# Performance work log

Hardware: AMD Instinct MI355X
Metric: run time of the kernel (lower is better)

Reference implementation:

```python
import jax, jax.numpy as jnp
import numpy as np

N, E, HID, HEADS, KHOPS = 10000, 160000, 64, 8, 3
D = HID // HEADS  # head_dim = 8


def setup_inputs() -> dict:
    key = jax.random.key(0)
    ks = jax.random.split(key, 8)
    s = 1.0 / np.sqrt(HID)
    return {
        "x": jax.random.normal(ks[0], (N, HID), jnp.float32),
        "edge_index": jax.random.randint(ks[1], (2, E), 0, N),
        "edge_feature": jax.random.normal(ks[2], (E, HID), jnp.float32),
        "edge_weight": jax.random.uniform(ks[3], (E,), jnp.float32),
        "Wq": jax.random.normal(ks[4], (HID, HID), jnp.float32) * s,
        "bq": jnp.zeros((HID,), jnp.float32),
        "Wk": jax.random.normal(ks[5], (HID, HID), jnp.float32) * s,
        "bk": jnp.zeros((HID,), jnp.float32),
        "Wv": jax.random.normal(ks[6], (HID, HID), jnp.float32) * s,
        "bv": jnp.zeros((HID,), jnp.float32),
        "hopwise": jnp.ones((KHOPS + 1,), jnp.float32),
    }


def reference(x, edge_index, edge_feature, edge_weight, Wq, bq, Wk, bk, Wv, bv, hopwise):
    n = x.shape[0]
    row, col = edge_index[0], edge_index[1]

    # symmetric degree normalization, scaled by edge_weight
    deg = jax.ops.segment_sum(jnp.ones_like(edge_weight), col, num_segments=n)
    deg_inv = jnp.where(deg > 0, deg ** -0.5, 0.0)
    norm = deg_inv[row] * deg_inv[col] * edge_weight  # [E]

    Q = jax.nn.relu(x @ Wq + bq).reshape(n, HEADS, D)
    K = (x @ Wk + bk).reshape(n, HEADS, D)
    V = (x @ Wv + bv).reshape(n, HEADS, D)
    ef = edge_feature.reshape(-1, HEADS, D)  # [E,h,d]

    hidden = V * hopwise[0]
    sqrt_d = jnp.sqrt(jnp.asarray(D, x.dtype))

    for hop in range(KHOPS):
        if hop == 0:
            Kj = jax.nn.relu(K[row] + ef)                 # [E,h,d]
            # per-edge K (x) V outer product message, scatter-summed at col
            msg = norm[:, None, None, None] * jnp.einsum('ehi,ehj->ehij', Kj, V[row])
            M = jax.ops.segment_sum(msg, col, num_segments=n)   # [N,h,d,d]
            K = jax.ops.segment_sum(norm[:, None, None] * Kj, col, num_segments=n)
        else:
            M = jax.ops.segment_sum(norm[:, None, None, None] * M[row], col, num_segments=n)
            K = jax.ops.segment_sum(norm[:, None, None] * K[row], col, num_segments=n)

        H = jnp.einsum('nhi,nhij->nhj', Q, M)             # [N,h,d]
        nrm = jnp.sqrt(jnp.sum((H / sqrt_d) ** 2, axis=-1))  # [N,h]
        H = H / jnp.maximum(jnp.ones_like(nrm), nrm)[..., None]
        hidden = hidden + hopwise[hop + 1] * H

    return hidden.reshape(n, HEADS * D)
```

## Files before the change

### kernel.cpp

```cpp
#include <hip/hip_runtime.h>
#include <hip/hip_bf16.h>


#define HIDC 64
#define MELEMS 512

__device__ __forceinline__ unsigned bf16rne(float x) {
    unsigned u = __float_as_uint(x);
    return (u + 0x7FFFu + ((u >> 16) & 1u)) >> 16;
}
__device__ __forceinline__ unsigned pack2(float lo, float hi) {
    return bf16rne(lo) | (bf16rne(hi) << 16);
}
__device__ __forceinline__ float bfval(unsigned short v) {
    return __uint_as_float((unsigned)v << 16);
}
__device__ __forceinline__ void acc8(float* acc, float s, uint4 a) {
    acc[0] = fmaf(s, __uint_as_float(a.x << 16), acc[0]);
    acc[1] = fmaf(s, __uint_as_float(a.x & 0xFFFF0000u), acc[1]);
    acc[2] = fmaf(s, __uint_as_float(a.y << 16), acc[2]);
    acc[3] = fmaf(s, __uint_as_float(a.y & 0xFFFF0000u), acc[3]);
    acc[4] = fmaf(s, __uint_as_float(a.z << 16), acc[4]);
    acc[5] = fmaf(s, __uint_as_float(a.z & 0xFFFF0000u), acc[5]);
    acc[6] = fmaf(s, __uint_as_float(a.w << 16), acc[6]);
    acc[7] = fmaf(s, __uint_as_float(a.w & 0xFFFF0000u), acc[7]);
}
__device__ __forceinline__ void fmaV(float* acc, float s, float4 a, float4 b) {
    acc[0] = fmaf(s, a.x, acc[0]); acc[1] = fmaf(s, a.y, acc[1]);
    acc[2] = fmaf(s, a.z, acc[2]); acc[3] = fmaf(s, a.w, acc[3]);
    acc[4] = fmaf(s, b.x, acc[4]); acc[5] = fmaf(s, b.y, acc[5]);
    acc[6] = fmaf(s, b.z, acc[6]); acc[7] = fmaf(s, b.w, acc[7]);
}

__global__ void qkv_kernel(const float* __restrict__ x,
                           const float* __restrict__ Wq, const float* __restrict__ bq,
                           const float* __restrict__ Wk, const float* __restrict__ bk,
                           const float* __restrict__ Wv, const float* __restrict__ bv,
                           const float* __restrict__ hopwise,
                           float* __restrict__ Q, float* __restrict__ K, float* __restrict__ V,
                           float* __restrict__ out, int* __restrict__ deg, int n) {
    int idx = blockIdx.x * blockDim.x + threadIdx.x;
    if (idx < n) deg[idx] = 0;
    if (idx >= n * HIDC) return;
    int node = idx >> 6, c = idx & 63;
    const float4* x4 = (const float4*)(x + (size_t)node * HIDC);
    float aq = bq[c], ak = bk[c], av = bv[c];
    #pragma unroll
    for (int k4 = 0; k4 < 16; ++k4) {
        float4 xv = x4[k4];
        int k = k4 * 4;
        aq = fmaf(xv.x, Wq[(k + 0) * HIDC + c], aq);
        ak = fmaf(xv.x, Wk[(k + 0) * HIDC + c], ak);
        av = fmaf(xv.x, Wv[(k + 0) * HIDC + c], av);
        aq = fmaf(xv.y, Wq[(k + 1) * HIDC + c], aq);
        ak = fmaf(xv.y, Wk[(k + 1) * HIDC + c], ak);
        av = fmaf(xv.y, Wv[(k + 1) * HIDC + c], av);
        aq = fmaf(xv.z, Wq[(k + 2) * HIDC + c], aq);
        ak = fmaf(xv.z, Wk[(k + 2) * HIDC + c], ak);
        av = fmaf(xv.z, Wv[(k + 2) * HIDC + c], av);
        aq = fmaf(xv.w, Wq[(k + 3) * HIDC + c], aq);
        ak = fmaf(xv.w, Wk[(k + 3) * HIDC + c], ak);
        av = fmaf(xv.w, Wv[(k + 3) * HIDC + c], av);
    }
    Q[idx] = fmaxf(aq, 0.f);
    K[idx] = ak;
    V[idx] = av;
    out[idx] = hopwise[0] * av;
}

__global__ void deg_kernel(const int* __restrict__ col, int* __restrict__ deg, int e) {
    int i = blockIdx.x * blockDim.x + threadIdx.x;
    if (i < e) atomicAdd(&deg[col[i]], 1);
}

__global__ __launch_bounds__(1024) void scan_kernel(const int* __restrict__ deg,
                                                    int* __restrict__ rowptr,
                                                    int* __restrict__ cursor, int n) {
    __shared__ int wsum[16];
    __shared__ int carry;
    int tid = threadIdx.x;
    int lane = tid & 63, w = tid >> 6;
    if (tid == 0) { carry = 0; rowptr[0] = 0; }
    __syncthreads();
    for (int start = 0; start < n; start += 1024) {
        int i = start + tid;
        int v = (i < n) ? deg[i] : 0;
        int s = v;
        #pragma unroll
        for (int off = 1; off < 64; off <<= 1) {
            int t = __shfl_up(s, off);
            if (lane >= off) s += t;
        }
        if (lane == 63) wsum[w] = s;
        __syncthreads();
        if (tid == 0) {
            int acc = carry;
            #pragma unroll
            for (int w2 = 0; w2 < 16; ++w2) { int t = wsum[w2]; wsum[w2] = acc; acc += t; }
            carry = acc;
        }
        __syncthreads();
        int incl = wsum[w] + s;
        if (i < n) {
            rowptr[i + 1] = incl;
            cursor[i] = incl - v;
        }
        __syncthreads();
    }
}

__global__ void pos_kernel(const int* __restrict__ row, const int* __restrict__ col,
                           const float* __restrict__ ew, const int* __restrict__ deg,
                           int* __restrict__ cursor,
                           int* __restrict__ srcrow, float* __restrict__ snorm,
                           int* __restrict__ posarr, int e) {
    int i = blockIdx.x * blockDim.x + threadIdx.x;
    if (i >= e) return;
    int r = row[i], c = col[i];
    int dr = deg[r], dc = deg[c];
    float nv = ew[i];
    nv *= (dr > 0) ? rsqrtf((float)dr) : 0.f;
    nv *= (dc > 0) ? rsqrtf((float)dc) : 0.f;
    int pos = atomicAdd(&cursor[c], 1);
    srcrow[pos] = r;
    snorm[pos] = nv;
    posarr[i] = pos;
}

__global__ __launch_bounds__(256) void kj_kernel(
    const int* __restrict__ row, const int* __restrict__ posarr,
    const float* __restrict__ K, const float* __restrict__ ef,
    unsigned short* __restrict__ kjb, int e) {
    int gtid = blockIdx.x * blockDim.x + threadIdx.x;
    int i = gtid >> 4;
    if (i >= e) return;
    int c4 = gtid & 15;
    int lane = threadIdx.x & 63;
    int lanebase = lane & 48;
    int r = 0, pos = 0;
    if (c4 == 0) { r = row[i]; pos = posarr[i]; }
    r = __shfl(r, lanebase);
    pos = __shfl(pos, lanebase);
    const float4* efv = (const float4*)ef;
    const float4* Kv = (const float4*)K;
    float4 f = efv[(size_t)i * 16 + c4];
    float4 kk = Kv[(size_t)r * 16 + c4];
    uint2 st;
    st.x = pack2(fmaxf(kk.x + f.x, 0.f), fmaxf(kk.y + f.y, 0.f));
    st.y = pack2(fmaxf(kk.z + f.z, 0.f), fmaxf(kk.w + f.w, 0.f));
    ((uint2*)kjb)[(size_t)pos * 16 + c4] = st;
}

__device__ __forceinline__ void epilogue64(const float* acc, const float* __restrict__ Q,
                                           float hw, int n, int h, int ii,
                                           float* __restrict__ out) {
    float q = Q[n * HIDC + h * 8 + ii];
    float p[8];
    #pragma unroll
    for (int j = 0; j < 8; ++j) p[j] = q * acc[j];
    #pragma unroll
    for (int off = 1; off < 8; off <<= 1) {
        #pragma unroll
        for (int j = 0; j < 8; ++j) p[j] += __shfl_xor(p[j], off);
    }
    float ssq = 0.f;
    #pragma unroll
    for (int j = 0; j < 8; ++j) ssq = fmaf(p[j], p[j], ssq);
    float nr = sqrtf(ssq * 0.125f);
    float sc = (nr > 1.f) ? (hw / nr) : hw;
    if (ii == 0) {
        float4* o = (float4*)(out + (size_t)n * HIDC + h * 8);
        float4 c0 = o[0], c1 = o[1];
        c0.x = fmaf(p[0], sc, c0.x); c0.y = fmaf(p[1], sc, c0.y);
        c0.z = fmaf(p[2], sc, c0.z); c0.w = fmaf(p[3], sc, c0.w);
        c1.x = fmaf(p[4], sc, c1.x); c1.y = fmaf(p[5], sc, c1.y);
        c1.z = fmaf(p[6], sc, c1.z); c1.w = fmaf(p[7], sc, c1.w);
        o[0] = c0; o[1] = c1;
    }
}

__global__ __launch_bounds__(256) void hop0_kernel(
    const int* __restrict__ rowptr, const int* __restrict__ srcrow,
    const float* __restrict__ snorm, const unsigned short* __restrict__ kjb,
    const float* __restrict__ V, const float* __restrict__ Q,
    const float* __restrict__ hopwise, unsigned short* __restrict__ M0,
    float* __restrict__ out, int nn) {
    int n = blockIdx.x * 4 + (threadIdx.x >> 6);
    if (n >= nn) return;
    int t = threadIdx.x & 63;
    int h = t >> 3, ii = t & 7;
    int beg = rowptr[n], end = rowptr[n + 1];
    float acc[8] = {0, 0, 0, 0, 0, 0, 0, 0};
    const float4* Vv = (const float4*)V;
    int k = beg;
    for (; k + 4 <= end; k += 4) {
        int j0 = srcrow[k], j1 = srcrow[k + 1], j2 = srcrow[k + 2], j3 = srcrow[k + 3];
        float s0 = snorm[k]     * bfval(kjb[(size_t)(k)     * HIDC + t]);
        float s1 = snorm[k + 1] * bfval(kjb[(size_t)(k + 1) * HIDC + t]);
        float s2 = snorm[k + 2] * bfval(kjb[(size_t)(k + 2) * HIDC + t]);
        float s3 = snorm[k + 3] * bfval(kjb[(size_t)(k + 3) * HIDC + t]);
        float4 a0 = Vv[j0 * 16 + h * 2], b0 = Vv[j0 * 16 + h * 2 + 1];
        float4 a1 = Vv[j1 * 16 + h * 2], b1 = Vv[j1 * 16 + h * 2 + 1];
        float4 a2 = Vv[j2 * 16 + h * 2], b2 = Vv[j2 * 16 + h * 2 + 1];
        float4 a3 = Vv[j3 * 16 + h * 2], b3 = Vv[j3 * 16 + h * 2 + 1];
        fmaV(acc, s0, a0, b0);
        fmaV(acc, s1, a1, b1);
        fmaV(acc, s2, a2, b2);
        fmaV(acc, s3, a3, b3);
    }
    for (; k < end; ++k) {
        int j = srcrow[k];
        float s = snorm[k] * bfval(kjb[(size_t)k * HIDC + t]);
        fmaV(acc, s, Vv[j * 16 + h * 2], Vv[j * 16 + h * 2 + 1]);
    }
    uint4 st;
    st.x = pack2(acc[0], acc[1]); st.y = pack2(acc[2], acc[3]);
    st.z = pack2(acc[4], acc[5]); st.w = pack2(acc[6], acc[7]);
    ((uint4*)M0)[(size_t)n * 64 + t] = st;
    epilogue64(acc, Q, hopwise[1], n, h, ii, out);
}

__global__ __launch_bounds__(256) void hopk_kernel(
    const int* __restrict__ rowptr, const int* __restrict__ srcrow,
    const float* __restrict__ snorm, const unsigned short* __restrict__ Min,
    const float* __restrict__ Q, const float* __restrict__ hopwise, int hopidx,
    unsigned short* __restrict__ Mout, int writeM, float* __restrict__ out, int nn) {
    int n = blockIdx.x * 4 + (threadIdx.x >> 6);
    if (n >= nn) return;
    int t = threadIdx.x & 63;
    int beg = rowptr[n], end = rowptr[n + 1];
    float acc[8] = {0, 0, 0, 0, 0, 0, 0, 0};
    const uint4* Mv = (const uint4*)Min;
    int k = beg;
    for (; k + 8 <= end; k += 8) {
        int j0 = srcrow[k],     j1 = srcrow[k + 1], j2 = srcrow[k + 2], j3 = srcrow[k + 3];
        int j4 = srcrow[k + 4], j5 = srcrow[k + 5], j6 = srcrow[k + 6], j7 = srcrow[k + 7];
        uint4 a0 = Mv[(size_t)j0 * 64 + t];
        uint4 a1 = Mv[(size_t)j1 * 64 + t];
        uint4 a2 = Mv[(size_t)j2 * 64 + t];
        uint4 a3 = Mv[(size_t)j3 * 64 + t];
        uint4 a4 = Mv[(size_t)j4 * 64 + t];
        uint4 a5 = Mv[(size_t)j5 * 64 + t];
        uint4 a6 = Mv[(size_t)j6 * 64 + t];
        uint4 a7 = Mv[(size_t)j7 * 64 + t];
        acc8(acc, snorm[k],     a0);
        acc8(acc, snorm[k + 1], a1);
        acc8(acc, snorm[k + 2], a2);
        acc8(acc, snorm[k + 3], a3);
        acc8(acc, snorm[k + 4], a4);
        acc8(acc, snorm[k + 5], a5);
        acc8(acc, snorm[k + 6], a6);
        acc8(acc, snorm[k + 7], a7);
    }
    for (; k + 4 <= end; k += 4) {
        int j0 = srcrow[k], j1 = srcrow[k + 1], j2 = srcrow[k + 2], j3 = srcrow[k + 3];
        uint4 a0 = Mv[(size_t)j0 * 64 + t];
        uint4 a1 = Mv[(size_t)j1 * 64 + t];
        uint4 a2 = Mv[(size_t)j2 * 64 + t];
        uint4 a3 = Mv[(size_t)j3 * 64 + t];
        acc8(acc, snorm[k],     a0);
        acc8(acc, snorm[k + 1], a1);
        acc8(acc, snorm[k + 2], a2);
        acc8(acc, snorm[k + 3], a3);
    }
    for (; k < end; ++k) acc8(acc, snorm[k], Mv[(size_t)srcrow[k] * 64 + t]);
    if (writeM) {
        uint4 st;
        st.x = pack2(acc[0], acc[1]); st.y = pack2(acc[2], acc[3]);
        st.z = pack2(acc[4], acc[5]); st.w = pack2(acc[6], acc[7]);
        ((uint4*)Mout)[(size_t)n * 64 + t] = st;
    }
    int h = t >> 3, ii = t & 7;
    epilogue64(acc, Q, hopwise[hopidx], n, h, ii, out);
}

extern "C" void kernel_launch(void* const* d_in, const int* in_sizes, int n_in,
                              void* d_out, int out_size, void* d_ws, size_t ws_size,
                              hipStream_t stream) {
    const float* x       = (const float*)d_in[0];
    const int*   ei      = (const int*)d_in[1];
    const float* ef      = (const float*)d_in[2];
    const float* ew      = (const float*)d_in[3];
    const float* Wq      = (const float*)d_in[4];
    const float* bq      = (const float*)d_in[5];
    const float* Wk      = (const float*)d_in[6];
    const float* bk      = (const float*)d_in[7];
    const float* Wv      = (const float*)d_in[8];
    const float* bv      = (const float*)d_in[9];
    const float* hopwise = (const float*)d_in[10];
    float* out = (float*)d_out;

    const int n = in_sizes[0] / HIDC;
    const int e = in_sizes[1] / 2;
    const int* row = ei;
    const int* col = ei + e;

    char* base = (char*)d_ws;
    size_t off = 0;
    auto alloc = [&](size_t bytes) -> void* {
        void* p = base + off;
        off = (off + bytes + 255) & ~(size_t)255;
        return p;
    };
    int*            deg    = (int*)           alloc((size_t)n * 4);
    int*            cursor = (int*)           alloc((size_t)n * 4);
    int*            rowptr = (int*)           alloc((size_t)(n + 1) * 4);
    int*            srcrow = (int*)           alloc((size_t)e * 4);
    float*          snorm  = (float*)         alloc((size_t)e * 4);
    int*            posarr = (int*)           alloc((size_t)e * 4);
    unsigned short* kjb    = (unsigned short*)alloc((size_t)e * HIDC * 2);
    float*          Q      = (float*)         alloc((size_t)n * HIDC * 4);
    float*          K      = (float*)         alloc((size_t)n * HIDC * 4);
    float*          V      = (float*)         alloc((size_t)n * HIDC * 4);
    unsigned short* M0     = (unsigned short*)alloc((size_t)n * MELEMS * 2);
    unsigned short* M1     = (unsigned short*)alloc((size_t)n * MELEMS * 2);
    (void)ws_size;

    int qb = (n * HIDC + 255) / 256;
    qkv_kernel<<<qb, 256, 0, stream>>>(x, Wq, bq, Wk, bk, Wv, bv, hopwise,
                                       Q, K, V, out, deg, n);

    int eb = (e + 255) / 256;
    deg_kernel<<<eb, 256, 0, stream>>>(col, deg, e);
    scan_kernel<<<1, 1024, 0, stream>>>(deg, rowptr, cursor, n);

    pos_kernel<<<eb, 256, 0, stream>>>(row, col, ew, deg, cursor,
                                       srcrow, snorm, posarr, e);
    int kb = ((e * 16) + 255) / 256;
    kj_kernel<<<kb, 256, 0, stream>>>(row, posarr, K, ef, kjb, e);

    int nb = (n + 3) / 4;
    hop0_kernel<<<nb, 256, 0, stream>>>(rowptr, srcrow, snorm, kjb, V, Q,
                                        hopwise, M0, out, n);
    hopk_kernel<<<nb, 256, 0, stream>>>(rowptr, srcrow, snorm, M0, Q, hopwise, 2, M1, 1, out, n);
    hopk_kernel<<<nb, 256, 0, stream>>>(rowptr, srcrow, snorm, M1, Q, hopwise, 3, M0, 0, out, n);
}
```

Baseline: 141.7 us.

## Replace serial scan with atomic block allocation and pre-gather V into edge buffer

The single-block serial prefix scan becomes a multi-block kernel. Each block scans locally and claims a base offset through an atomic counter, so segments are contiguous per node but no longer globally ordered, and rowptr is replaced by rowbeg plus deg. The kj kernel now also gathers V[row] as bf16 next to Kj in a 128-element per-edge record, so hop0 reads contiguous data instead of gathering V in fp32. This adds write traffic for the extra V copy and introduces V rounding to bf16.

```diff
diff --git a/kernel.cpp b/kernel.cpp
--- a/kernel.cpp
+++ b/kernel.cpp
@@ -25,12 +25,6 @@
     acc[6] = fmaf(s, __uint_as_float(a.w << 16), acc[6]);
     acc[7] = fmaf(s, __uint_as_float(a.w & 0xFFFF0000u), acc[7]);
 }
-__device__ __forceinline__ void fmaV(float* acc, float s, float4 a, float4 b) {
-    acc[0] = fmaf(s, a.x, acc[0]); acc[1] = fmaf(s, a.y, acc[1]);
-    acc[2] = fmaf(s, a.z, acc[2]); acc[3] = fmaf(s, a.w, acc[3]);
-    acc[4] = fmaf(s, b.x, acc[4]); acc[5] = fmaf(s, b.y, acc[5]);
-    acc[6] = fmaf(s, b.z, acc[6]); acc[7] = fmaf(s, b.w, acc[7]);
-}
 
 __global__ void qkv_kernel(const float* __restrict__ x,
                            const float* __restrict__ Wq, const float* __restrict__ bq,
@@ -38,9 +32,11 @@
                            const float* __restrict__ Wv, const float* __restrict__ bv,
                            const float* __restrict__ hopwise,
                            float* __restrict__ Q, float* __restrict__ K, float* __restrict__ V,
-                           float* __restrict__ out, int* __restrict__ deg, int n) {
+                           float* __restrict__ out, int* __restrict__ deg,
+                           int* __restrict__ counter, int n) {
     int idx = blockIdx.x * blockDim.x + threadIdx.x;
     if (idx < n) deg[idx] = 0;
+    if (idx == 0) *counter = 0;
     if (idx >= n * HIDC) return;
     int node = idx >> 6, c = idx & 63;
     const float4* x4 = (const float4*)(x + (size_t)node * HIDC);
@@ -73,39 +69,34 @@
     if (i < e) atomicAdd(&deg[col[i]], 1);
 }
 
-__global__ __launch_bounds__(1024) void scan_kernel(const int* __restrict__ deg,
-                                                    int* __restrict__ rowptr,
+__global__ __launch_bounds__(1024) void base_kernel(const int* __restrict__ deg,
+                                                    int* __restrict__ counter,
+                                                    int* __restrict__ rowbeg,
                                                     int* __restrict__ cursor, int n) {
     __shared__ int wsum[16];
-    __shared__ int carry;
-    int tid = threadIdx.x;
-    int lane = tid & 63, w = tid >> 6;
-    if (tid == 0) { carry = 0; rowptr[0] = 0; }
+    __shared__ int blockbase;
+    int i = blockIdx.x * 1024 + threadIdx.x;
+    int lane = threadIdx.x & 63, w = threadIdx.x >> 6;
+    int v = (i < n) ? deg[i] : 0;
+    int s = v;
+    #pragma unroll
+    for (int off = 1; off < 64; off <<= 1) {
+        int t = __shfl_up(s, off);
+        if (lane >= off) s += t;
+    }
+    if (lane == 63) wsum[w] = s;
     __syncthreads();
-    for (int start = 0; start < n; start += 1024) {
-        int i = start + tid;
-        int v = (i < n) ? deg[i] : 0;
-        int s = v;
+    if (threadIdx.x == 0) {
+        int acc = 0;
         #pragma unroll
-        for (int off = 1; off < 64; off <<= 1) {
-            int t = __shfl_up(s, off);
-            if (lane >= off) s += t;
-        }
-        if (lane == 63) wsum[w] = s;
-        __syncthreads();
-        if (tid == 0) {
-            int acc = carry;
-            #pragma unroll
-            for (int w2 = 0; w2 < 16; ++w2) { int t = wsum[w2]; wsum[w2] = acc; acc += t; }
-            carry = acc;
-        }
-        __syncthreads();
-        int incl = wsum[w] + s;
-        if (i < n) {
-            rowptr[i + 1] = incl;
-            cursor[i] = incl - v;
-        }
-        __syncthreads();
+        for (int w2 = 0; w2 < 16; ++w2) { int t = wsum[w2]; wsum[w2] = acc; acc += t; }
+        blockbase = atomicAdd(counter, acc);
+    }
+    __syncthreads();
+    int excl = blockbase + wsum[w] + s - v;
+    if (i < n) {
+        rowbeg[i] = excl;
+        cursor[i] = excl;
     }
 }
 
@@ -127,28 +118,33 @@
     posarr[i] = pos;
 }
 
-__global__ __launch_bounds__(256) void kj_kernel(
+__global__ __launch_bounds__(256) void kjv_kernel(
     const int* __restrict__ row, const int* __restrict__ posarr,
-    const float* __restrict__ K, const float* __restrict__ ef,
-    unsigned short* __restrict__ kjb, int e) {
+    const float* __restrict__ K, const float* __restrict__ V,
+    const float* __restrict__ ef, unsigned short* __restrict__ kjv, int e) {
     int gtid = blockIdx.x * blockDim.x + threadIdx.x;
     int i = gtid >> 4;
     if (i >= e) return;
     int c4 = gtid & 15;
-    int lane = threadIdx.x & 63;
-    int lanebase = lane & 48;
+    int lanebase = (threadIdx.x & 63) & 48;
     int r = 0, pos = 0;
     if (c4 == 0) { r = row[i]; pos = posarr[i]; }
     r = __shfl(r, lanebase);
     pos = __shfl(pos, lanebase);
     const float4* efv = (const float4*)ef;
     const float4* Kv = (const float4*)K;
+    const float4* Vv = (const float4*)V;
     float4 f = efv[(size_t)i * 16 + c4];
     float4 kk = Kv[(size_t)r * 16 + c4];
-    uint2 st;
-    st.x = pack2(fmaxf(kk.x + f.x, 0.f), fmaxf(kk.y + f.y, 0.f));
-    st.y = pack2(fmaxf(kk.z + f.z, 0.f), fmaxf(kk.w + f.w, 0.f));
-    ((uint2*)kjb)[(size_t)pos * 16 + c4] = st;
+    float4 vv = Vv[(size_t)r * 16 + c4];
+    uint2 kjp, vp;
+    kjp.x = pack2(fmaxf(kk.x + f.x, 0.f), fmaxf(kk.y + f.y, 0.f));
+    kjp.y = pack2(fmaxf(kk.z + f.z, 0.f), fmaxf(kk.w + f.w, 0.f));
+    vp.x = pack2(vv.x, vv.y);
+    vp.y = pack2(vv.z, vv.w);
+    uint2* rowp = (uint2*)(kjv + (size_t)pos * 128);
+    rowp[c4] = kjp;
+    rowp[16 + c4] = vp;
 }
 
 __device__ __forceinline__ void epilogue64(const float* acc, const float* __restrict__ Q,
@@ -180,38 +176,35 @@
 }
 
 __global__ __launch_bounds__(256) void hop0_kernel(
-    const int* __restrict__ rowptr, const int* __restrict__ srcrow,
-    const float* __restrict__ snorm, const unsigned short* __restrict__ kjb,
-    const float* __restrict__ V, const float* __restrict__ Q,
-    const float* __restrict__ hopwise, unsigned short* __restrict__ M0,
-    float* __restrict__ out, int nn) {
+    const int* __restrict__ rowbeg, const int* __restrict__ deg,
+    const float* __restrict__ snorm, const unsigned short* __restrict__ kjv,
+    const float* __restrict__ Q, const float* __restrict__ hopwise,
+    unsigned short* __restrict__ M0, float* __restrict__ out, int nn) {
     int n = blockIdx.x * 4 + (threadIdx.x >> 6);
     if (n >= nn) return;
     int t = threadIdx.x & 63;
     int h = t >> 3, ii = t & 7;
-    int beg = rowptr[n], end = rowptr[n + 1];
+    int beg = rowbeg[n], end = beg + deg[n];
     float acc[8] = {0, 0, 0, 0, 0, 0, 0, 0};
-    const float4* Vv = (const float4*)V;
     int k = beg;
     for (; k + 4 <= end; k += 4) {
-        int j0 = srcrow[k], j1 = srcrow[k + 1], j2 = srcrow[k + 2], j3 = srcrow[k + 3];
-        float s0 = snorm[k]     * bfval(kjb[(size_t)(k)     * HIDC + t]);
-        float s1 = snorm[k + 1] * bfval(kjb[(size_t)(k + 1) * HIDC + t]);
-        float s2 = snorm[k + 2] * bfval(kjb[(size_t)(k + 2) * HIDC + t]);
-        float s3 = snorm[k + 3] * bfval(kjb[(size_t)(k + 3) * HIDC + t]);
-        float4 a0 = Vv[j0 * 16 + h * 2], b0 = Vv[j0 * 16 + h * 2 + 1];
-        float4 a1 = Vv[j1 * 16 + h * 2], b1 = Vv[j1 * 16 + h * 2 + 1];
-        float4 a2 = Vv[j2 * 16 + h * 2], b2 = Vv[j2 * 16 + h * 2 + 1];
-        float4 a3 = Vv[j3 * 16 + h * 2], b3 = Vv[j3 * 16 + h * 2 + 1];
-        fmaV(acc, s0, a0, b0);
-        fmaV(acc, s1, a1, b1);
-        fmaV(acc, s2, a2, b2);
-        fmaV(acc, s3, a3, b3);
+        float s0 = snorm[k]     * bfval(kjv[(size_t)(k)     * 128 + t]);
+        float s1 = snorm[k + 1] * bfval(kjv[(size_t)(k + 1) * 128 + t]);
+        float s2 = snorm[k + 2] * bfval(kjv[(size_t)(k + 2) * 128 + t]);
+        float s3 = snorm[k + 3] * bfval(kjv[(size_t)(k + 3) * 128 + t]);
+        uint4 v0 = *(const uint4*)(kjv + (size_t)(k)     * 128 + 64 + h * 8);
+        uint4 v1 = *(const uint4*)(kjv + (size_t)(k + 1) * 128 + 64 + h * 8);
+        uint4 v2 = *(const uint4*)(kjv + (size_t)(k + 2) * 128 + 64 + h * 8);
+        uint4 v3 = *(const uint4*)(kjv + (size_t)(k + 3) * 128 + 64 + h * 8);
+        acc8(acc, s0, v0);
+        acc8(acc, s1, v1);
+        acc8(acc, s2, v2);
+        acc8(acc, s3, v3);
     }
     for (; k < end; ++k) {
-        int j = srcrow[k];
-        float s = snorm[k] * bfval(kjb[(size_t)k * HIDC + t]);
-        fmaV(acc, s, Vv[j * 16 + h * 2], Vv[j * 16 + h * 2 + 1]);
+        float s = snorm[k] * bfval(kjv[(size_t)k * 128 + t]);
+        uint4 v = *(const uint4*)(kjv + (size_t)k * 128 + 64 + h * 8);
+        acc8(acc, s, v);
     }
     uint4 st;
     st.x = pack2(acc[0], acc[1]); st.y = pack2(acc[2], acc[3]);
@@ -221,14 +214,15 @@
 }
 
 __global__ __launch_bounds__(256) void hopk_kernel(
-    const int* __restrict__ rowptr, const int* __restrict__ srcrow,
-    const float* __restrict__ snorm, const unsigned short* __restrict__ Min,
-    const float* __restrict__ Q, const float* __restrict__ hopwise, int hopidx,
+    const int* __restrict__ rowbeg, const int* __restrict__ deg,
+    const int* __restrict__ srcrow, const float* __restrict__ snorm,
+    const unsigned short* __restrict__ Min, const float* __restrict__ Q,
+    const float* __restrict__ hopwise, int hopidx,
     unsigned short* __restrict__ Mout, int writeM, float* __restrict__ out, int nn) {
     int n = blockIdx.x * 4 + (threadIdx.x >> 6);
     if (n >= nn) return;
     int t = threadIdx.x & 63;
-    int beg = rowptr[n], end = rowptr[n + 1];
+    int beg = rowbeg[n], end = beg + deg[n];
     float acc[8] = {0, 0, 0, 0, 0, 0, 0, 0};
     const uint4* Mv = (const uint4*)Min;
     int k = beg;
@@ -302,36 +296,39 @@
         off = (off + bytes + 255) & ~(size_t)255;
         return p;
     };
-    int*            deg    = (int*)           alloc((size_t)n * 4);
-    int*            cursor = (int*)           alloc((size_t)n * 4);
-    int*            rowptr = (int*)           alloc((size_t)(n + 1) * 4);
-    int*            srcrow = (int*)           alloc((size_t)e * 4);
-    float*          snorm  = (float*)         alloc((size_t)e * 4);
-    int*            posarr = (int*)           alloc((size_t)e * 4);
-    unsigned short* kjb    = (unsigned short*)alloc((size_t)e * HIDC * 2);
-    float*          Q      = (float*)         alloc((size_t)n * HIDC * 4);
-    float*          K      = (float*)         alloc((size_t)n * HIDC * 4);
-    float*          V      = (float*)         alloc((size_t)n * HIDC * 4);
-    unsigned short* M0     = (unsigned short*)alloc((size_t)n * MELEMS * 2);
-    unsigned short* M1     = (unsigned short*)alloc((size_t)n * MELEMS * 2);
+    int*            deg     = (int*)           alloc((size_t)n * 4);
+    int*            cursor  = (int*)           alloc((size_t)n * 4);
+    int*            rowbeg  = (int*)           alloc((size_t)n * 4);
+    int*            counter = (int*)           alloc(256);
+    int*            srcrow  = (int*)           alloc((size_t)e * 4);
+    float*          snorm   = (float*)         alloc((size_t)e * 4);
+    int*            posarr  = (int*)           alloc((size_t)e * 4);
+    unsigned short* kjv     = (unsigned short*)alloc((size_t)e * 128 * 2);
+    float*          Q       = (float*)         alloc((size_t)n * HIDC * 4);
+    float*          K       = (float*)         alloc((size_t)n * HIDC * 4);
+    float*          V       = (float*)         alloc((size_t)n * HIDC * 4);
+    unsigned short* M0      = (unsigned short*)alloc((size_t)n * MELEMS * 2);
+    unsigned short* M1      = (unsigned short*)alloc((size_t)n * MELEMS * 2);
     (void)ws_size;
 
     int qb = (n * HIDC + 255) / 256;
     qkv_kernel<<<qb, 256, 0, stream>>>(x, Wq, bq, Wk, bk, Wv, bv, hopwise,
-                                       Q, K, V, out, deg, n);
+                                       Q, K, V, out, deg, counter, n);
 
     int eb = (e + 255) / 256;
     deg_kernel<<<eb, 256, 0, stream>>>(col, deg, e);
-    scan_kernel<<<1, 1024, 0, stream>>>(deg, rowptr, cursor, n);
+
+    int bb = (n + 1023) / 1024;
+    base_kernel<<<bb, 1024, 0, stream>>>(deg, counter, rowbeg, cursor, n);
 
     pos_kernel<<<eb, 256, 0, stream>>>(row, col, ew, deg, cursor,
                                        srcrow, snorm, posarr, e);
+
     int kb = ((e * 16) + 255) / 256;
-    kj_kernel<<<kb, 256, 0, stream>>>(row, posarr, K, ef, kjb, e);
+    kjv_kernel<<<kb, 256, 0, stream>>>(row, posarr, K, V, ef, kjv, e);
 
     int nb = (n + 3) / 4;
-    hop0_kernel<<<nb, 256, 0, stream>>>(rowptr, srcrow, snorm, kjb, V, Q,
-                                        hopwise, M0, out, n);
-    hopk_kernel<<<nb, 256, 0, stream>>>(rowptr, srcrow, snorm, M0, Q, hopwise, 2, M1, 1, out, n);
-    hopk_kernel<<<nb, 256, 0, stream>>>(rowptr, srcrow, snorm, M1, Q, hopwise, 3, M0, 0, out, n);
-}
+    hop0_kernel<<<nb, 256, 0, stream>>>(rowbeg, deg, snorm, kjv, Q, hopwise, M0, out, n);
+    hopk_kernel<<<nb, 256, 0, stream>>>(rowbeg, deg, srcrow, snorm, M0, Q, hopwise, 2, M1, 1, out, n);
+    hopk_kernel<<<nb, 256, 0, stream>>>(rowbeg, deg, srcrow, snorm, M1, Q, hopwise, 3, M0, 0, out, n);
+}
```

Result: faster. 134.4 us (-5.1%).
